# Kernel tuning notes

Measured on AMD Instinct MI355X. Metric: run time of the kernel, lower is better.

Reference implementation:

```python
import jax, jax.numpy as jnp
import numpy as np

H = 64  # hidden_size


def lstm_layer(x, Wih, Whh, bih, bhh):
    """Single LSTM layer, batch_first input x: [B, T, D]. Returns (hs [B,T,H], h_last [B,H]).
    PyTorch gate order: i, f, g, o."""
    B, T, _ = x.shape
    # Precompute input projections for all timesteps: [T, B, 4H]
    xg = jnp.einsum('btd,gd->tbg', x, Wih) + (bih + bhh)

    def step(carry, xt):
        h, c = carry
        gates = xt + h @ Whh.T  # [B, 4H]
        i, f, g, o = jnp.split(gates, 4, axis=-1)
        i = jax.nn.sigmoid(i)
        f = jax.nn.sigmoid(f)
        g = jnp.tanh(g)
        o = jax.nn.sigmoid(o)
        c = f * c + i * g
        h = o * jnp.tanh(c)
        return (h, c), h

    h0 = jnp.zeros((B, H), dtype=x.dtype)
    c0 = jnp.zeros((B, H), dtype=x.dtype)
    (h_last, _), hs = jax.lax.scan(step, (h0, c0), xg)
    return jnp.transpose(hs, (1, 0, 2)), h_last  # [B,T,H], [B,H]


def setup_inputs() -> dict:
    key = jax.random.key(0)
    ks = jax.random.split(key, 11)
    B, T, D = 1024, 512, 6
    s0 = 1.0 / np.sqrt(H)
    u = lambda k, shp: jax.random.uniform(k, shp, jnp.float32, -s0, s0)
    return {
        'x': jax.random.normal(ks[0], (B, T, D), jnp.float32),
        'Wih0': u(ks[1], (4 * H, D)),
        'Whh0': u(ks[2], (4 * H, H)),
        'bih0': u(ks[3], (4 * H,)),
        'bhh0': u(ks[4], (4 * H,)),
        'Wih1': u(ks[5], (4 * H, H)),
        'Whh1': u(ks[6], (4 * H, H)),
        'bih1': u(ks[7], (4 * H,)),
        'bhh1': u(ks[8], (4 * H,)),
        'W1': u(ks[9], (32, H)),
        'b1': jnp.zeros((32,), jnp.float32),
        'W2': u(ks[10], (1, 32)),
        'b2': jnp.zeros((1,), jnp.float32),
    }


def reference(x, Wih0, Whh0, bih0, bhh0, Wih1, Whh1, bih1, bhh1, W1, b1, W2, b2):
    # Layer 0 (dropout between layers is identity in eval mode)
    hs0, _ = lstm_layer(x, Wih0, Whh0, bih0, bhh0)
    # Layer 1: only last hidden state needed
    _, h_last = lstm_layer(hs0, Wih1, Whh1, bih1, bhh1)
    # MLP head: Linear -> ReLU -> (Dropout=identity) -> Linear -> Sigmoid
    z = jax.nn.relu(h_last @ W1.T + b1)
    out = jax.nn.sigmoid(z @ W2.T + b2)
    return out.squeeze()  # [B]
```

## Files before the change

kernel.cpp:

```cpp
#include <hip/hip_runtime.h>
#include <cstdint>

#define Hh 64
#define Tt 512
#define Dd 6
#define BB 4
#define NT 512

typedef short bf16x8 __attribute__((ext_vector_type(8)));
typedef float f32x4  __attribute__((ext_vector_type(4)));

#define MF(A, B, C) C = __builtin_amdgcn_mfma_f32_16x16x32_bf16(A, B, C, 0, 0, 0)

__device__ __forceinline__ float sigm(float v){
  return __builtin_amdgcn_rcpf(1.f + __expf(-v));
}
__device__ __forceinline__ float tanh_(float v){
  return 1.f - 2.f*__builtin_amdgcn_rcpf(1.f + __expf(2.f*v));
}
__device__ __forceinline__ unsigned short f2bf(float f){
  union { float f; unsigned u; } v; v.f = f;
  unsigned r = v.u + 0x7FFFu + ((v.u >> 16) & 1u);
  return (unsigned short)(r >> 16);
}
__device__ __forceinline__ float bf2f(unsigned short b){
  union { unsigned u; float f; } v; v.u = ((unsigned)b) << 16;
  return v.f;
}
__device__ __forceinline__ void split8(const float* w, bf16x8& hi, bf16x8& lo){
  #pragma unroll
  for (int i = 0; i < 8; ++i){
    unsigned short h_ = f2bf(w[i]);
    hi[i] = (short)h_;
    lo[i] = (short)f2bf(w[i] - bf2f(h_));
  }
}

__global__ __launch_bounds__(NT, 2)
void lstm2_mfma(const float* __restrict__ x,
                const float* __restrict__ Wih0, const float* __restrict__ Whh0,
                const float* __restrict__ bih0, const float* __restrict__ bhh0,
                const float* __restrict__ Wih1, const float* __restrict__ Whh1,
                const float* __restrict__ bih1, const float* __restrict__ bhh1,
                const float* __restrict__ W1, const float* __restrict__ b1,
                const float* __restrict__ W2, const float* __restrict__ b2,
                float* __restrict__ out)
{
  __shared__ __align__(16) short hsb[2*2*1024];
  __shared__ __align__(16) float h1f[BB*Hh];
  __shared__ float zs[BB*32];

  const int tid  = threadIdx.x;
  const int lane = tid & 63;
  const int wid  = tid >> 6;
  const int lr   = lane & 15;
  const int lg   = lane >> 4;
  const int b0   = blockIdx.x * BB;

  const int u_l  = lr >> 3;
  const int u_p  = (lr >> 2) & 1;
  const int u_bs = lr & 3;
  const int u_j  = wid*8 + u_p*4 + lg;

  {
    int* hz = (int*)hsb;
    hz[tid] = 0; hz[tid+NT] = 0; hz[tid+2*NT] = 0; hz[tid+3*NT] = 0;
  }

  bf16x8 A0[2][2][2];
  bf16x8 A1[2][2][2][2];
  #pragma unroll
  for (int p = 0; p < 2; ++p){
    const int m = (lr&3)*64 + wid*8 + p*4 + (lr>>2);
    #pragma unroll
    for (int kt = 0; kt < 2; ++kt){
      const int off = m*64 + kt*32 + lg*8;
      float wbuf[8];
      *(float4*)&wbuf[0] = *(const float4*)&Whh0[off];
      *(float4*)&wbuf[4] = *(const float4*)&Whh0[off+4];
      split8(wbuf, A0[p][kt][0], A0[p][kt][1]);
      *(float4*)&wbuf[0] = *(const float4*)&Wih1[off];
      *(float4*)&wbuf[4] = *(const float4*)&Wih1[off+4];
      split8(wbuf, A1[p][0][kt][0], A1[p][0][kt][1]);
      *(float4*)&wbuf[0] = *(const float4*)&Whh1[off];
      *(float4*)&wbuf[4] = *(const float4*)&Whh1[off+4];
      split8(wbuf, A1[p][1][kt][0], A1[p][1][kt][1]);
    }
  }

  float bias_g[4], w0r[24];
  #pragma unroll
  for (int gt = 0; gt < 4; ++gt){
    const int row = gt*64 + u_j;
    if (u_l == 0){
      bias_g[gt] = bih0[row] + bhh0[row];
      #pragma unroll
      for (int d = 0; d < Dd; ++d) w0r[gt*6+d] = Wih0[row*Dd + d];
    } else {
      bias_g[gt] = bih1[row] + bhh1[row];
      #pragma unroll
      for (int d = 0; d < Dd; ++d) w0r[gt*6+d] = 0.f;
    }
  }

  const int boff0 = (lr*128 + lg*16)      ^ ((lr&7)<<4);
  const int boff1 = (lr*128 + 64 + lg*16) ^ ((lr&7)<<4);
  const int whi   = (u_bs*128     + u_j*2) ^ (u_bs<<4);
  const int wlo   = ((u_bs+4)*128 + u_j*2) ^ ((u_bs+4)<<4);

  const float2* px2 = (const float2*)(x + (size_t)(b0 + u_bs) * (Tt*Dd));
  float2 xi0 = px2[0], xi1 = px2[1], xi2 = px2[2];
  float2 xc0 = px2[3], xc1 = px2[4], xc2 = px2[5];
  float2 xf0 = px2[6], xf1 = px2[7], xf2 = px2[8];

  float creg = 0.f;
  __syncthreads();

  if (u_l == 0){
    float s[4];
    #pragma unroll
    for (int gt = 0; gt < 4; ++gt)
      s[gt] = bias_g[gt] + w0r[gt*6+0]*xi0.x + w0r[gt*6+1]*xi0.y
            + w0r[gt*6+2]*xi1.x + w0r[gt*6+3]*xi1.y
            + w0r[gt*6+4]*xi2.x + w0r[gt*6+5]*xi2.y;
    float iv = sigm(s[0]), fv = sigm(s[1]), gv = tanh_(s[2]), ov = sigm(s[3]);
    creg = fv*creg + iv*gv;
    float hval = ov * tanh_(creg);
    unsigned short hh = f2bf(hval);
    unsigned short hl = f2bf(hval - bf2f(hh));
    char* hw = (char*)hsb;
    *(short*)(hw + whi) = (short)hh;
    *(short*)(hw + wlo) = (short)hl;
  }
  __syncthreads();

  #pragma unroll 2
  for (int t = 0; t < Tt; ++t){
    float2 xn0, xn1, xn2;
    {
      const int tl = (t+3 < Tt) ? (t+3) : (Tt-1);
      xn0 = px2[tl*3]; xn1 = px2[tl*3+1]; xn2 = px2[tl*3+2];
    }

    const int buf = t & 1;
    const char* hb = (const char*)hsb + buf*4096;
    bf16x8 b00 = *(const bf16x8*)(hb + boff0);
    bf16x8 b01 = *(const bf16x8*)(hb + boff1);
    bf16x8 b10 = *(const bf16x8*)(hb + 2048 + boff0);
    bf16x8 b11 = *(const bf16x8*)(hb + 2048 + boff1);

    f32x4 a00 = {0,0,0,0}, a01 = {0,0,0,0}, a10 = {0,0,0,0}, a11 = {0,0,0,0};
    MF(A0[0][0][0], b00, a00); MF(A0[1][0][0], b00, a01);
    MF(A0[0][1][0], b01, a00); MF(A0[1][1][0], b01, a01);
    MF(A0[0][0][1], b00, a00); MF(A0[1][0][1], b00, a01);
    MF(A0[0][1][1], b01, a00); MF(A0[1][1][1], b01, a01);

    float g0[4];
    #pragma unroll
    for (int rg = 0; rg < 4; ++rg){
      float own = (lr & 4) ? a01[rg] : a00[rg];
      float snd = (lr & 4) ? a00[rg] : a01[rg];
      g0[rg] = own + __shfl_xor(snd, 4);
    }

    MF(A1[0][0][0][0], b00, a10); MF(A1[1][0][0][0], b00, a11);
    MF(A1[0][0][1][0], b01, a10); MF(A1[1][0][1][0], b01, a11);
    MF(A1[0][0][0][1], b00, a10); MF(A1[1][0][0][1], b00, a11);
    MF(A1[0][0][1][1], b01, a10); MF(A1[1][0][1][1], b01, a11);
    MF(A1[0][1][0][0], b10, a10); MF(A1[1][1][0][0], b10, a11);
    MF(A1[0][1][1][0], b11, a10); MF(A1[1][1][1][0], b11, a11);
    MF(A1[0][1][0][1], b10, a10); MF(A1[1][1][0][1], b10, a11);
    MF(A1[0][1][1][1], b11, a10); MF(A1[1][1][1][1], b11, a11);

    float g1[4];
    #pragma unroll
    for (int rg = 0; rg < 4; ++rg){
      float s10 = a10[rg] + __shfl_xor(a10[rg], 4);
      float s11 = a11[rg] + __shfl_xor(a11[rg], 4);
      float snd = (lr & 4) ? s11 : s10;
      g1[rg] = __shfl_xor(snd, 8);
    }

    if ((u_l == 1) | (t+1 < Tt)){
      float s0 = ((u_l == 0) ? g0[0] : g1[0]) + bias_g[0];
      float s1 = ((u_l == 0) ? g0[1] : g1[1]) + bias_g[1];
      float s2 = ((u_l == 0) ? g0[2] : g1[2]) + bias_g[2];
      float s3 = ((u_l == 0) ? g0[3] : g1[3]) + bias_g[3];
      if (u_l == 0){
        s0 += w0r[ 0]*xc0.x + w0r[ 1]*xc0.y + w0r[ 2]*xc1.x
            + w0r[ 3]*xc1.y + w0r[ 4]*xc2.x + w0r[ 5]*xc2.y;
        s1 += w0r[ 6]*xc0.x + w0r[ 7]*xc0.y + w0r[ 8]*xc1.x
            + w0r[ 9]*xc1.y + w0r[10]*xc2.x + w0r[11]*xc2.y;
        s2 += w0r[12]*xc0.x + w0r[13]*xc0.y + w0r[14]*xc1.x
            + w0r[15]*xc1.y + w0r[16]*xc2.x + w0r[17]*xc2.y;
        s3 += w0r[18]*xc0.x + w0r[19]*xc0.y + w0r[20]*xc1.x
            + w0r[21]*xc1.y + w0r[22]*xc2.x + w0r[23]*xc2.y;
      }
      float iv = sigm(s0), fv = sigm(s1), gv = tanh_(s2), ov = sigm(s3);
      creg = fv*creg + iv*gv;
      float hval = ov * tanh_(creg);
      if ((u_l == 1) & (t == Tt-1)) h1f[u_bs*64 + u_j] = hval;
      unsigned short hh = f2bf(hval);
      unsigned short hl = f2bf(hval - bf2f(hh));
      char* hw = (char*)hsb + (buf^1)*4096 + u_l*2048;
      *(short*)(hw + whi) = (short)hh;
      *(short*)(hw + wlo) = (short)hl;
    }

    xc0 = xf0; xc1 = xf1; xc2 = xf2;
    xf0 = xn0; xf1 = xn1; xf2 = xn2;

    __syncthreads();
  }

  if (tid < BB*32){
    const int bsh = tid >> 5, m = tid & 31;
    float acc = b1[m];
    #pragma unroll
    for (int j = 0; j < Hh; ++j) acc += W1[m*Hh + j] * h1f[bsh*64 + j];
    zs[bsh*32 + m] = fmaxf(acc, 0.f);
  }
  __syncthreads();
  if (tid < BB){
    float acc = b2[0];
    #pragma unroll
    for (int m = 0; m < 32; ++m) acc += W2[m] * zs[tid*32 + m];
    out[b0 + tid] = sigm(acc);
  }
}

extern "C" void kernel_launch(void* const* d_in, const int* in_sizes, int n_in,
                              void* d_out, int out_size, void* d_ws, size_t ws_size,
                              hipStream_t stream) {
  const float* x    = (const float*)d_in[0];
  const float* Wih0 = (const float*)d_in[1];
  const float* Whh0 = (const float*)d_in[2];
  const float* bih0 = (const float*)d_in[3];
  const float* bhh0 = (const float*)d_in[4];
  const float* Wih1 = (const float*)d_in[5];
  const float* Whh1 = (const float*)d_in[6];
  const float* bih1 = (const float*)d_in[7];
  const float* bhh1 = (const float*)d_in[8];
  const float* W1   = (const float*)d_in[9];
  const float* b1   = (const float*)d_in[10];
  const float* W2   = (const float*)d_in[11];
  const float* b2   = (const float*)d_in[12];

  const int B = in_sizes[0] / (Tt*Dd);
  dim3 grid(B / BB), block(NT);
  hipLaunchKernelGGL(lstm2_mfma, grid, block, 0, stream,
                     x, Wih0, Whh0, bih0, bhh0, Wih1, Whh1, bih1, bhh1,
                     W1, b1, W2, b2, (float*)d_out);
}
```

Before: 436.0 us.

## Halve block to four waves, each lane computing both LSTM layers' units

Cuts the block from 512 to 256 threads. Each wave now owns 16 hidden units instead of 8 and holds weight fragments for both layers. Every lane runs the cell update for layer 0 and layer 1, instead of splitting lanes between layers. Layer-1 input and recurrent products go into separate accumulators and are summed before the cross-lane shuffle reduction. The aim is fewer waves taking part in each per-timestep barrier and less lane divergence, at the cost of more register pressure (launch bounds lowered to 1) and more serial MFMA and transcendental work per wave.

After: 770.0 us. +76.6%, slower.

```diff
diff --git a/kernel.cpp b/kernel.cpp
--- a/kernel.cpp
+++ b/kernel.cpp
@@ -5,7 +5,7 @@
 #define Tt 512
 #define Dd 6
 #define BB 4
-#define NT 512
+#define NT 256
 
 typedef short bf16x8 __attribute__((ext_vector_type(8)));
 typedef float f32x4  __attribute__((ext_vector_type(4)));
@@ -36,7 +36,7 @@
   }
 }
 
-__global__ __launch_bounds__(NT, 2)
+__global__ __launch_bounds__(NT, 1)
 void lstm2_mfma(const float* __restrict__ x,
                 const float* __restrict__ Wih0, const float* __restrict__ Whh0,
                 const float* __restrict__ bih0, const float* __restrict__ bhh0,
@@ -55,23 +55,24 @@
   const int wid  = tid >> 6;
   const int lr   = lane & 15;
   const int lg   = lane >> 4;
+  const int sb2  = (lr >> 2) & 1;
+  const int sb3  = lr >> 3;
+  const int u_bs = lr & 3;
+  const int u_j  = wid*16 + (2*sb3 + sb2)*4 + lg;
   const int b0   = blockIdx.x * BB;
-
-  const int u_l  = lr >> 3;
-  const int u_p  = (lr >> 2) & 1;
-  const int u_bs = lr & 3;
-  const int u_j  = wid*8 + u_p*4 + lg;
 
   {
     int* hz = (int*)hsb;
-    hz[tid] = 0; hz[tid+NT] = 0; hz[tid+2*NT] = 0; hz[tid+3*NT] = 0;
-  }
-
-  bf16x8 A0[2][2][2];
-  bf16x8 A1[2][2][2][2];
+    #pragma unroll
+    for (int i = 0; i < 8; ++i) hz[tid + i*NT] = 0;
+  }
+
+  bf16x8 A0[4][2][2];
+  bf16x8 A1i[4][2][2];
+  bf16x8 A1h[4][2][2];
   #pragma unroll
-  for (int p = 0; p < 2; ++p){
-    const int m = (lr&3)*64 + wid*8 + p*4 + (lr>>2);
+  for (int p = 0; p < 4; ++p){
+    const int m = (lr&3)*64 + wid*16 + p*4 + (lr>>2);
     #pragma unroll
     for (int kt = 0; kt < 2; ++kt){
       const int off = m*64 + kt*32 + lg*8;
@@ -81,26 +82,21 @@
       split8(wbuf, A0[p][kt][0], A0[p][kt][1]);
       *(float4*)&wbuf[0] = *(const float4*)&Wih1[off];
       *(float4*)&wbuf[4] = *(const float4*)&Wih1[off+4];
-      split8(wbuf, A1[p][0][kt][0], A1[p][0][kt][1]);
+      split8(wbuf, A1i[p][kt][0], A1i[p][kt][1]);
       *(float4*)&wbuf[0] = *(const float4*)&Whh1[off];
       *(float4*)&wbuf[4] = *(const float4*)&Whh1[off+4];
-      split8(wbuf, A1[p][1][kt][0], A1[p][1][kt][1]);
-    }
-  }
-
-  float bias_g[4], w0r[24];
+      split8(wbuf, A1h[p][kt][0], A1h[p][kt][1]);
+    }
+  }
+
+  float bias0g[4], bias1g[4], w0r[24];
   #pragma unroll
   for (int gt = 0; gt < 4; ++gt){
     const int row = gt*64 + u_j;
-    if (u_l == 0){
-      bias_g[gt] = bih0[row] + bhh0[row];
-      #pragma unroll
-      for (int d = 0; d < Dd; ++d) w0r[gt*6+d] = Wih0[row*Dd + d];
-    } else {
-      bias_g[gt] = bih1[row] + bhh1[row];
-      #pragma unroll
-      for (int d = 0; d < Dd; ++d) w0r[gt*6+d] = 0.f;
-    }
+    bias0g[gt] = bih0[row] + bhh0[row];
+    bias1g[gt] = bih1[row] + bhh1[row];
+    #pragma unroll
+    for (int d = 0; d < Dd; ++d) w0r[gt*6+d] = Wih0[row*Dd + d];
   }
 
   const int boff0 = (lr*128 + lg*16)      ^ ((lr&7)<<4);
@@ -113,19 +109,19 @@
   float2 xc0 = px2[3], xc1 = px2[4], xc2 = px2[5];
   float2 xf0 = px2[6], xf1 = px2[7], xf2 = px2[8];
 
-  float creg = 0.f;
+  float c0reg = 0.f, c1reg = 0.f;
   __syncthreads();
 
-  if (u_l == 0){
+  {
     float s[4];
     #pragma unroll
     for (int gt = 0; gt < 4; ++gt)
-      s[gt] = bias_g[gt] + w0r[gt*6+0]*xi0.x + w0r[gt*6+1]*xi0.y
+      s[gt] = bias0g[gt] + w0r[gt*6+0]*xi0.x + w0r[gt*6+1]*xi0.y
             + w0r[gt*6+2]*xi1.x + w0r[gt*6+3]*xi1.y
             + w0r[gt*6+4]*xi2.x + w0r[gt*6+5]*xi2.y;
     float iv = sigm(s[0]), fv = sigm(s[1]), gv = tanh_(s[2]), ov = sigm(s[3]);
-    creg = fv*creg + iv*gv;
-    float hval = ov * tanh_(creg);
+    c0reg = fv*c0reg + iv*gv;
+    float hval = ov * tanh_(c0reg);
     unsigned short hh = f2bf(hval);
     unsigned short hl = f2bf(hval - bf2f(hh));
     char* hw = (char*)hsb;
@@ -149,60 +145,89 @@
     bf16x8 b10 = *(const bf16x8*)(hb + 2048 + boff0);
     bf16x8 b11 = *(const bf16x8*)(hb + 2048 + boff1);
 
-    f32x4 a00 = {0,0,0,0}, a01 = {0,0,0,0}, a10 = {0,0,0,0}, a11 = {0,0,0,0};
-    MF(A0[0][0][0], b00, a00); MF(A0[1][0][0], b00, a01);
-    MF(A0[0][1][0], b01, a00); MF(A0[1][1][0], b01, a01);
-    MF(A0[0][0][1], b00, a00); MF(A0[1][0][1], b00, a01);
-    MF(A0[0][1][1], b01, a00); MF(A0[1][1][1], b01, a01);
-
-    float g0[4];
+    f32x4 a0_[4], a1i_[4], a1h_[4];
+    #pragma unroll
+    for (int p = 0; p < 4; ++p){
+      a0_[p] = (f32x4){0,0,0,0}; a1i_[p] = (f32x4){0,0,0,0}; a1h_[p] = (f32x4){0,0,0,0};
+    }
+    #pragma unroll
+    for (int p = 0; p < 4; ++p){
+      MF(A0[p][0][0], b00, a0_[p]);
+      MF(A0[p][1][0], b01, a0_[p]);
+      MF(A0[p][0][1], b00, a0_[p]);
+      MF(A0[p][1][1], b01, a0_[p]);
+    }
+    #pragma unroll
+    for (int p = 0; p < 4; ++p){
+      MF(A1i[p][0][0], b00, a1i_[p]);
+      MF(A1i[p][1][0], b01, a1i_[p]);
+      MF(A1i[p][0][1], b00, a1i_[p]);
+      MF(A1i[p][1][1], b01, a1i_[p]);
+    }
+    #pragma unroll
+    for (int p = 0; p < 4; ++p){
+      MF(A1h[p][0][0], b10, a1h_[p]);
+      MF(A1h[p][1][0], b11, a1h_[p]);
+      MF(A1h[p][0][1], b10, a1h_[p]);
+      MF(A1h[p][1][1], b11, a1h_[p]);
+    }
+
+    float g0[4], g1[4];
     #pragma unroll
     for (int rg = 0; rg < 4; ++rg){
-      float own = (lr & 4) ? a01[rg] : a00[rg];
-      float snd = (lr & 4) ? a00[rg] : a01[rg];
-      g0[rg] = own + __shfl_xor(snd, 4);
-    }
-
-    MF(A1[0][0][0][0], b00, a10); MF(A1[1][0][0][0], b00, a11);
-    MF(A1[0][0][1][0], b01, a10); MF(A1[1][0][1][0], b01, a11);
-    MF(A1[0][0][0][1], b00, a10); MF(A1[1][0][0][1], b00, a11);
-    MF(A1[0][0][1][1], b01, a10); MF(A1[1][0][1][1], b01, a11);
-    MF(A1[0][1][0][0], b10, a10); MF(A1[1][1][0][0], b10, a11);
-    MF(A1[0][1][1][0], b11, a10); MF(A1[1][1][1][0], b11, a11);
-    MF(A1[0][1][0][1], b10, a10); MF(A1[1][1][0][1], b10, a11);
-    MF(A1[0][1][1][1], b11, a10); MF(A1[1][1][1][1], b11, a11);
-
-    float g1[4];
-    #pragma unroll
-    for (int rg = 0; rg < 4; ++rg){
-      float s10 = a10[rg] + __shfl_xor(a10[rg], 4);
-      float s11 = a11[rg] + __shfl_xor(a11[rg], 4);
-      float snd = (lr & 4) ? s11 : s10;
-      g1[rg] = __shfl_xor(snd, 8);
-    }
-
-    if ((u_l == 1) | (t+1 < Tt)){
-      float s0 = ((u_l == 0) ? g0[0] : g1[0]) + bias_g[0];
-      float s1 = ((u_l == 0) ? g0[1] : g1[1]) + bias_g[1];
-      float s2 = ((u_l == 0) ? g0[2] : g1[2]) + bias_g[2];
-      float s3 = ((u_l == 0) ? g0[3] : g1[3]) + bias_g[3];
-      if (u_l == 0){
-        s0 += w0r[ 0]*xc0.x + w0r[ 1]*xc0.y + w0r[ 2]*xc1.x
-            + w0r[ 3]*xc1.y + w0r[ 4]*xc2.x + w0r[ 5]*xc2.y;
-        s1 += w0r[ 6]*xc0.x + w0r[ 7]*xc0.y + w0r[ 8]*xc1.x
-            + w0r[ 9]*xc1.y + w0r[10]*xc2.x + w0r[11]*xc2.y;
-        s2 += w0r[12]*xc0.x + w0r[13]*xc0.y + w0r[14]*xc1.x
-            + w0r[15]*xc1.y + w0r[16]*xc2.x + w0r[17]*xc2.y;
-        s3 += w0r[18]*xc0.x + w0r[19]*xc0.y + w0r[20]*xc1.x
-            + w0r[21]*xc1.y + w0r[22]*xc2.x + w0r[23]*xc2.y;
-      }
+      float own  = sb2 ? a0_[1][rg] : a0_[0][rg];
+      float snd  = sb2 ? a0_[0][rg] : a0_[1][rg];
+      float own2 = sb2 ? a0_[3][rg] : a0_[2][rg];
+      float snd2 = sb2 ? a0_[2][rg] : a0_[3][rg];
+      float f  = own  + __shfl_xor(snd, 4);
+      float f2 = own2 + __shfl_xor(snd2, 4);
+      g0[rg] = sb3 ? __shfl_xor(f2, 8) : f;
+      float m0 = a1i_[0][rg] + a1h_[0][rg];
+      float m1 = a1i_[1][rg] + a1h_[1][rg];
+      float m2 = a1i_[2][rg] + a1h_[2][rg];
+      float m3 = a1i_[3][rg] + a1h_[3][rg];
+      float o1  = sb2 ? m1 : m0, s1_ = sb2 ? m0 : m1;
+      float o2_ = sb2 ? m3 : m2, s2_ = sb2 ? m2 : m3;
+      float h_  = o1  + __shfl_xor(s1_, 4);
+      float h2_ = o2_ + __shfl_xor(s2_, 4);
+      g1[rg] = sb3 ? __shfl_xor(h2_, 8) : h_;
+    }
+
+    if (t+1 < Tt){
+      float s0 = g0[0] + bias0g[0]
+               + w0r[ 0]*xc0.x + w0r[ 1]*xc0.y + w0r[ 2]*xc1.x
+               + w0r[ 3]*xc1.y + w0r[ 4]*xc2.x + w0r[ 5]*xc2.y;
+      float s1 = g0[1] + bias0g[1]
+               + w0r[ 6]*xc0.x + w0r[ 7]*xc0.y + w0r[ 8]*xc1.x
+               + w0r[ 9]*xc1.y + w0r[10]*xc2.x + w0r[11]*xc2.y;
+      float s2 = g0[2] + bias0g[2]
+               + w0r[12]*xc0.x + w0r[13]*xc0.y + w0r[14]*xc1.x
+               + w0r[15]*xc1.y + w0r[16]*xc2.x + w0r[17]*xc2.y;
+      float s3 = g0[3] + bias0g[3]
+               + w0r[18]*xc0.x + w0r[19]*xc0.y + w0r[20]*xc1.x
+               + w0r[21]*xc1.y + w0r[22]*xc2.x + w0r[23]*xc2.y;
       float iv = sigm(s0), fv = sigm(s1), gv = tanh_(s2), ov = sigm(s3);
-      creg = fv*creg + iv*gv;
-      float hval = ov * tanh_(creg);
-      if ((u_l == 1) & (t == Tt-1)) h1f[u_bs*64 + u_j] = hval;
+      c0reg = fv*c0reg + iv*gv;
+      float hval = ov * tanh_(c0reg);
       unsigned short hh = f2bf(hval);
       unsigned short hl = f2bf(hval - bf2f(hh));
-      char* hw = (char*)hsb + (buf^1)*4096 + u_l*2048;
+      char* hw = (char*)hsb + (buf^1)*4096;
+      *(short*)(hw + whi) = (short)hh;
+      *(short*)(hw + wlo) = (short)hl;
+    }
+
+    {
+      float s0 = g1[0] + bias1g[0];
+      float s1 = g1[1] + bias1g[1];
+      float s2 = g1[2] + bias1g[2];
+      float s3 = g1[3] + bias1g[3];
+      float iv = sigm(s0), fv = sigm(s1), gv = tanh_(s2), ov = sigm(s3);
+      c1reg = fv*c1reg + iv*gv;
+      float hval = ov * tanh_(c1reg);
+      if (t == Tt-1) h1f[u_bs*64 + u_j] = hval;
+      unsigned short hh = f2bf(hval);
+      unsigned short hl = f2bf(hval - bf2f(hh));
+      char* hw = (char*)hsb + (buf^1)*4096 + 2048;
       *(short*)(hw + whi) = (short)hh;
       *(short*)(hw + wlo) = (short)hl;
     }
```

## Process eight sequences per block with 16 waves and split gate work across lanes

Applied to the files above, without the earlier changes.

Doubles the batch per block to 8 sequences and the block to 1024 threads, with each wave owning 4 hidden units instead of 8. Per-wave MFMA work drops to 12 instructions per step in three independent accumulator chains, and the input projection is split across lane halves and exchanged with a shuffle. The aim is a shorter serial latency per timestep on the recurrent critical path. The cost is half as many blocks, occupancy limited to one block per CU, and a barrier across 16 waves each step.

Result: slower. 577.5 us (+32.4%).

```diff
diff --git a/kernel.cpp b/kernel.cpp
--- a/kernel.cpp
+++ b/kernel.cpp
@@ -4,8 +4,8 @@
 #define Hh 64
 #define Tt 512
 #define Dd 6
-#define BB 4
-#define NT 512
+#define BB 8
+#define NT 1024
 
 typedef short bf16x8 __attribute__((ext_vector_type(8)));
 typedef float f32x4  __attribute__((ext_vector_type(4)));
@@ -36,7 +36,7 @@
   }
 }
 
-__global__ __launch_bounds__(NT, 2)
+__global__ __launch_bounds__(NT, 1)
 void lstm2_mfma(const float* __restrict__ x,
                 const float* __restrict__ Wih0, const float* __restrict__ Whh0,
                 const float* __restrict__ bih0, const float* __restrict__ bhh0,
@@ -55,82 +55,82 @@
   const int wid  = tid >> 6;
   const int lr   = lane & 15;
   const int lg   = lane >> 4;
+  const int u_l  = (lane >> 3) & 1;
+  const int u_bs = lane & 7;
+  const int u_j  = wid*4 + lg;
   const int b0   = blockIdx.x * BB;
-
-  const int u_l  = lr >> 3;
-  const int u_p  = (lr >> 2) & 1;
-  const int u_bs = lr & 3;
-  const int u_j  = wid*8 + u_p*4 + lg;
 
   {
     int* hz = (int*)hsb;
-    hz[tid] = 0; hz[tid+NT] = 0; hz[tid+2*NT] = 0; hz[tid+3*NT] = 0;
-  }
-
-  bf16x8 A0[2][2][2];
-  bf16x8 A1[2][2][2][2];
-  #pragma unroll
-  for (int p = 0; p < 2; ++p){
-    const int m = (lr&3)*64 + wid*8 + p*4 + (lr>>2);
+    #pragma unroll
+    for (int i = 0; i < 4; ++i) hz[tid + i*NT] = 0;
+  }
+
+  bf16x8 A0[2][2];
+  bf16x8 A1i[2][2];
+  bf16x8 A1h[2][2];
+  {
+    const int m = (lr&3)*64 + wid*4 + (lr>>2);
     #pragma unroll
     for (int kt = 0; kt < 2; ++kt){
       const int off = m*64 + kt*32 + lg*8;
       float wbuf[8];
       *(float4*)&wbuf[0] = *(const float4*)&Whh0[off];
       *(float4*)&wbuf[4] = *(const float4*)&Whh0[off+4];
-      split8(wbuf, A0[p][kt][0], A0[p][kt][1]);
+      split8(wbuf, A0[kt][0], A0[kt][1]);
       *(float4*)&wbuf[0] = *(const float4*)&Wih1[off];
       *(float4*)&wbuf[4] = *(const float4*)&Wih1[off+4];
-      split8(wbuf, A1[p][0][kt][0], A1[p][0][kt][1]);
+      split8(wbuf, A1i[kt][0], A1i[kt][1]);
       *(float4*)&wbuf[0] = *(const float4*)&Whh1[off];
       *(float4*)&wbuf[4] = *(const float4*)&Whh1[off+4];
-      split8(wbuf, A1[p][1][kt][0], A1[p][1][kt][1]);
-    }
-  }
-
-  float bias_g[4], w0r[24];
+      split8(wbuf, A1h[kt][0], A1h[kt][1]);
+    }
+  }
+
+  float bias_g[4], w0r[12];
   #pragma unroll
   for (int gt = 0; gt < 4; ++gt){
     const int row = gt*64 + u_j;
-    if (u_l == 0){
-      bias_g[gt] = bih0[row] + bhh0[row];
-      #pragma unroll
-      for (int d = 0; d < Dd; ++d) w0r[gt*6+d] = Wih0[row*Dd + d];
-    } else {
-      bias_g[gt] = bih1[row] + bhh1[row];
-      #pragma unroll
-      for (int d = 0; d < Dd; ++d) w0r[gt*6+d] = 0.f;
-    }
+    bias_g[gt] = (u_l == 0) ? (bih0[row] + bhh0[row]) : (bih1[row] + bhh1[row]);
+  }
+  #pragma unroll
+  for (int e = 0; e < 2; ++e){
+    const int row = (2*u_l + e)*64 + u_j;
+    #pragma unroll
+    for (int d = 0; d < Dd; ++d) w0r[e*6+d] = Wih0[row*Dd + d];
   }
 
   const int boff0 = (lr*128 + lg*16)      ^ ((lr&7)<<4);
   const int boff1 = (lr*128 + 64 + lg*16) ^ ((lr&7)<<4);
   const int whi   = (u_bs*128     + u_j*2) ^ (u_bs<<4);
-  const int wlo   = ((u_bs+4)*128 + u_j*2) ^ ((u_bs+4)<<4);
+  const int wlo   = ((u_bs+8)*128 + u_j*2) ^ (u_bs<<4);
 
   const float2* px2 = (const float2*)(x + (size_t)(b0 + u_bs) * (Tt*Dd));
-  float2 xi0 = px2[0], xi1 = px2[1], xi2 = px2[2];
   float2 xc0 = px2[3], xc1 = px2[4], xc2 = px2[5];
   float2 xf0 = px2[6], xf1 = px2[7], xf2 = px2[8];
 
   float creg = 0.f;
   __syncthreads();
 
-  if (u_l == 0){
-    float s[4];
-    #pragma unroll
-    for (int gt = 0; gt < 4; ++gt)
-      s[gt] = bias_g[gt] + w0r[gt*6+0]*xi0.x + w0r[gt*6+1]*xi0.y
-            + w0r[gt*6+2]*xi1.x + w0r[gt*6+3]*xi1.y
-            + w0r[gt*6+4]*xi2.x + w0r[gt*6+5]*xi2.y;
-    float iv = sigm(s[0]), fv = sigm(s[1]), gv = tanh_(s[2]), ov = sigm(s[3]);
-    creg = fv*creg + iv*gv;
-    float hval = ov * tanh_(creg);
-    unsigned short hh = f2bf(hval);
-    unsigned short hl = f2bf(hval - bf2f(hh));
-    char* hw = (char*)hsb;
-    *(short*)(hw + whi) = (short)hh;
-    *(short*)(hw + wlo) = (short)hl;
+  {
+    float2 xi0 = px2[0], xi1 = px2[1], xi2 = px2[2];
+    float xpA = w0r[0]*xi0.x + w0r[1]*xi0.y + w0r[2]*xi1.x
+              + w0r[3]*xi1.y + w0r[4]*xi2.x + w0r[5]*xi2.y;
+    float xpB = w0r[6]*xi0.x + w0r[7]*xi0.y + w0r[8]*xi1.x
+              + w0r[9]*xi1.y + w0r[10]*xi2.x + w0r[11]*xi2.y;
+    float r2 = __shfl_xor(xpA, 8), r3 = __shfl_xor(xpB, 8);
+    if (u_l == 0){
+      float s0 = bias_g[0] + xpA, s1 = bias_g[1] + xpB;
+      float s2 = bias_g[2] + r2,  s3 = bias_g[3] + r3;
+      float iv = sigm(s0), fv = sigm(s1), gv = tanh_(s2), ov = sigm(s3);
+      creg = fv*creg + iv*gv;
+      float hval = ov * tanh_(creg);
+      unsigned short hh = f2bf(hval);
+      unsigned short hl = f2bf(hval - bf2f(hh));
+      char* hw = (char*)hsb;
+      *(short*)(hw + whi) = (short)hh;
+      *(short*)(hw + wlo) = (short)hl;
+    }
   }
   __syncthreads();
 
@@ -149,53 +149,33 @@
     bf16x8 b10 = *(const bf16x8*)(hb + 2048 + boff0);
     bf16x8 b11 = *(const bf16x8*)(hb + 2048 + boff1);
 
-    f32x4 a00 = {0,0,0,0}, a01 = {0,0,0,0}, a10 = {0,0,0,0}, a11 = {0,0,0,0};
-    MF(A0[0][0][0], b00, a00); MF(A0[1][0][0], b00, a01);
-    MF(A0[0][1][0], b01, a00); MF(A0[1][1][0], b01, a01);
-    MF(A0[0][0][1], b00, a00); MF(A0[1][0][1], b00, a01);
-    MF(A0[0][1][1], b01, a00); MF(A0[1][1][1], b01, a01);
-
-    float g0[4];
-    #pragma unroll
-    for (int rg = 0; rg < 4; ++rg){
-      float own = (lr & 4) ? a01[rg] : a00[rg];
-      float snd = (lr & 4) ? a00[rg] : a01[rg];
-      g0[rg] = own + __shfl_xor(snd, 4);
-    }
-
-    MF(A1[0][0][0][0], b00, a10); MF(A1[1][0][0][0], b00, a11);
-    MF(A1[0][0][1][0], b01, a10); MF(A1[1][0][1][0], b01, a11);
-    MF(A1[0][0][0][1], b00, a10); MF(A1[1][0][0][1], b00, a11);
-    MF(A1[0][0][1][1], b01, a10); MF(A1[1][0][1][1], b01, a11);
-    MF(A1[0][1][0][0], b10, a10); MF(A1[1][1][0][0], b10, a11);
-    MF(A1[0][1][1][0], b11, a10); MF(A1[1][1][1][0], b11, a11);
-    MF(A1[0][1][0][1], b10, a10); MF(A1[1][1][0][1], b10, a11);
-    MF(A1[0][1][1][1], b11, a10); MF(A1[1][1][1][1], b11, a11);
-
-    float g1[4];
-    #pragma unroll
-    for (int rg = 0; rg < 4; ++rg){
-      float s10 = a10[rg] + __shfl_xor(a10[rg], 4);
-      float s11 = a11[rg] + __shfl_xor(a11[rg], 4);
-      float snd = (lr & 4) ? s11 : s10;
-      g1[rg] = __shfl_xor(snd, 8);
-    }
+    f32x4 a0 = {0,0,0,0}, a1i = {0,0,0,0}, a1h = {0,0,0,0};
+    MF(A0[0][0], b00, a0);  MF(A1i[0][0], b00, a1i);  MF(A1h[0][0], b10, a1h);
+    MF(A0[1][0], b01, a0);  MF(A1i[1][0], b01, a1i);  MF(A1h[1][0], b11, a1h);
+    MF(A0[0][1], b00, a0);  MF(A1i[0][1], b00, a1i);  MF(A1h[0][1], b10, a1h);
+    MF(A0[1][1], b01, a0);  MF(A1i[1][1], b01, a1i);  MF(A1h[1][1], b11, a1h);
+
+    float xpA = w0r[0]*xc0.x + w0r[1]*xc0.y + w0r[2]*xc1.x
+              + w0r[3]*xc1.y + w0r[4]*xc2.x + w0r[5]*xc2.y;
+    float xpB = w0r[6]*xc0.x + w0r[7]*xc0.y + w0r[8]*xc1.x
+              + w0r[9]*xc1.y + w0r[10]*xc2.x + w0r[11]*xc2.y;
+    float r2 = __shfl_xor(xpA, 8), r3 = __shfl_xor(xpB, 8);
+
+    float s0, s1, s2, s3;
+    {
+      float m0 = a1i[0] + a1h[0], m1 = a1i[1] + a1h[1],
+            m2 = a1i[2] + a1h[2], m3 = a1i[3] + a1h[3];
+      float q0 = u_l ? m0 : a0[0], q1 = u_l ? m1 : a0[1],
+            q2 = u_l ? m2 : a0[2], q3 = u_l ? m3 : a0[3];
+      s0 = q0 + __shfl_xor(u_l ? m0 : a0[0], 8);
+      s1 = q1 + __shfl_xor(u_l ? m1 : a0[1], 8);
+      s2 = q2 + __shfl_xor(u_l ? m2 : a0[2], 8);
+      s3 = q3 + __shfl_xor(u_l ? m3 : a0[3], 8);
+    }
+    s0 += bias_g[0]; s1 += bias_g[1]; s2 += bias_g[2]; s3 += bias_g[3];
+    if (u_l == 0){ s0 += xpA; s1 += xpB; s2 += r2; s3 += r3; }
 
     if ((u_l == 1) | (t+1 < Tt)){
-      float s0 = ((u_l == 0) ? g0[0] : g1[0]) + bias_g[0];
-      float s1 = ((u_l == 0) ? g0[1] : g1[1]) + bias_g[1];
-      float s2 = ((u_l == 0) ? g0[2] : g1[2]) + bias_g[2];
-      float s3 = ((u_l == 0) ? g0[3] : g1[3]) + bias_g[3];
-      if (u_l == 0){
-        s0 += w0r[ 0]*xc0.x + w0r[ 1]*xc0.y + w0r[ 2]*xc1.x
-            + w0r[ 3]*xc1.y + w0r[ 4]*xc2.x + w0r[ 5]*xc2.y;
-        s1 += w0r[ 6]*xc0.x + w0r[ 7]*xc0.y + w0r[ 8]*xc1.x
-            + w0r[ 9]*xc1.y + w0r[10]*xc2.x + w0r[11]*xc2.y;
-        s2 += w0r[12]*xc0.x + w0r[13]*xc0.y + w0r[14]*xc1.x
-            + w0r[15]*xc1.y + w0r[16]*xc2.x + w0r[17]*xc2.y;
-        s3 += w0r[18]*xc0.x + w0r[19]*xc0.y + w0r[20]*xc1.x
-            + w0r[21]*xc1.y + w0r[22]*xc2.x + w0r[23]*xc2.y;
-      }
       float iv = sigm(s0), fv = sigm(s1), gv = tanh_(s2), ov = sigm(s3);
       creg = fv*creg + iv*gv;
       float hval = ov * tanh_(creg);
```

## Issue all MFMAs upfront, split layer gate paths, truncate bf16 split, lighter barrier

Applied to the files above, without the earlier changes.

Issues both layers' MFMAs together and splits the layer-1 accumulators into separate input and hidden chains, so the layer-0 reduction and gate math can overlap with the layer-1 MFMAs. The layer-0 and layer-1 gate evaluations become separate branches instead of one select-based shared path. The rounding bf16 hi/lo split becomes plain truncation, and the loop barrier becomes an inline s_waitcnt lgkmcnt(0) plus s_barrier. Launch bounds drop from 2 to 1 block per SM, which gives more registers per thread but may lower occupancy.

New measurement: 540.0 us. 23.9% more time.

```diff
diff --git a/kernel.cpp b/kernel.cpp
--- a/kernel.cpp
+++ b/kernel.cpp
@@ -35,8 +35,15 @@
     lo[i] = (short)f2bf(w[i] - bf2f(h_));
   }
 }
-
-__global__ __launch_bounds__(NT, 2)
+__device__ __forceinline__ void splitH(float v, unsigned short& hh, unsigned short& hl){
+  union { float f; unsigned u; } a; a.f = v;
+  hh = (unsigned short)(a.u >> 16);
+  float resid = v - bf2f(hh);
+  union { float f; unsigned u; } b; b.f = resid;
+  hl = (unsigned short)(b.u >> 16);
+}
+
+__global__ __launch_bounds__(NT, 1)
 void lstm2_mfma(const float* __restrict__ x,
                 const float* __restrict__ Wih0, const float* __restrict__ Whh0,
                 const float* __restrict__ bih0, const float* __restrict__ bhh0,
@@ -126,8 +133,7 @@
     float iv = sigm(s[0]), fv = sigm(s[1]), gv = tanh_(s[2]), ov = sigm(s[3]);
     creg = fv*creg + iv*gv;
     float hval = ov * tanh_(creg);
-    unsigned short hh = f2bf(hval);
-    unsigned short hl = f2bf(hval - bf2f(hh));
+    unsigned short hh, hl; splitH(hval, hh, hl);
     char* hw = (char*)hsb;
     *(short*)(hw + whi) = (short)hh;
     *(short*)(hw + wlo) = (short)hl;
@@ -149,11 +155,22 @@
     bf16x8 b10 = *(const bf16x8*)(hb + 2048 + boff0);
     bf16x8 b11 = *(const bf16x8*)(hb + 2048 + boff1);
 
-    f32x4 a00 = {0,0,0,0}, a01 = {0,0,0,0}, a10 = {0,0,0,0}, a11 = {0,0,0,0};
+    f32x4 a00  = {0,0,0,0}, a01  = {0,0,0,0};
+    f32x4 a1iA = {0,0,0,0}, a1iB = {0,0,0,0};
+    f32x4 a1hA = {0,0,0,0}, a1hB = {0,0,0,0};
+
     MF(A0[0][0][0], b00, a00); MF(A0[1][0][0], b00, a01);
     MF(A0[0][1][0], b01, a00); MF(A0[1][1][0], b01, a01);
     MF(A0[0][0][1], b00, a00); MF(A0[1][0][1], b00, a01);
     MF(A0[0][1][1], b01, a00); MF(A0[1][1][1], b01, a01);
+    MF(A1[0][0][0][0], b00, a1iA); MF(A1[1][0][0][0], b00, a1iB);
+    MF(A1[0][0][1][0], b01, a1iA); MF(A1[1][0][1][0], b01, a1iB);
+    MF(A1[0][0][0][1], b00, a1iA); MF(A1[1][0][0][1], b00, a1iB);
+    MF(A1[0][0][1][1], b01, a1iA); MF(A1[1][0][1][1], b01, a1iB);
+    MF(A1[0][1][0][0], b10, a1hA); MF(A1[1][1][0][0], b10, a1hB);
+    MF(A1[0][1][1][0], b11, a1hA); MF(A1[1][1][1][0], b11, a1hB);
+    MF(A1[0][1][0][1], b10, a1hA); MF(A1[1][1][0][1], b10, a1hB);
+    MF(A1[0][1][1][1], b11, a1hA); MF(A1[1][1][1][1], b11, a1hB);
 
     float g0[4];
     #pragma unroll
@@ -162,56 +179,60 @@
       float snd = (lr & 4) ? a00[rg] : a01[rg];
       g0[rg] = own + __shfl_xor(snd, 4);
     }
-
-    MF(A1[0][0][0][0], b00, a10); MF(A1[1][0][0][0], b00, a11);
-    MF(A1[0][0][1][0], b01, a10); MF(A1[1][0][1][0], b01, a11);
-    MF(A1[0][0][0][1], b00, a10); MF(A1[1][0][0][1], b00, a11);
-    MF(A1[0][0][1][1], b01, a10); MF(A1[1][0][1][1], b01, a11);
-    MF(A1[0][1][0][0], b10, a10); MF(A1[1][1][0][0], b10, a11);
-    MF(A1[0][1][1][0], b11, a10); MF(A1[1][1][1][0], b11, a11);
-    MF(A1[0][1][0][1], b10, a10); MF(A1[1][1][0][1], b10, a11);
-    MF(A1[0][1][1][1], b11, a10); MF(A1[1][1][1][1], b11, a11);
-
-    float g1[4];
-    #pragma unroll
-    for (int rg = 0; rg < 4; ++rg){
-      float s10 = a10[rg] + __shfl_xor(a10[rg], 4);
-      float s11 = a11[rg] + __shfl_xor(a11[rg], 4);
-      float snd = (lr & 4) ? s11 : s10;
-      g1[rg] = __shfl_xor(snd, 8);
-    }
-
-    if ((u_l == 1) | (t+1 < Tt)){
-      float s0 = ((u_l == 0) ? g0[0] : g1[0]) + bias_g[0];
-      float s1 = ((u_l == 0) ? g0[1] : g1[1]) + bias_g[1];
-      float s2 = ((u_l == 0) ? g0[2] : g1[2]) + bias_g[2];
-      float s3 = ((u_l == 0) ? g0[3] : g1[3]) + bias_g[3];
-      if (u_l == 0){
-        s0 += w0r[ 0]*xc0.x + w0r[ 1]*xc0.y + w0r[ 2]*xc1.x
-            + w0r[ 3]*xc1.y + w0r[ 4]*xc2.x + w0r[ 5]*xc2.y;
-        s1 += w0r[ 6]*xc0.x + w0r[ 7]*xc0.y + w0r[ 8]*xc1.x
-            + w0r[ 9]*xc1.y + w0r[10]*xc2.x + w0r[11]*xc2.y;
-        s2 += w0r[12]*xc0.x + w0r[13]*xc0.y + w0r[14]*xc1.x
-            + w0r[15]*xc1.y + w0r[16]*xc2.x + w0r[17]*xc2.y;
-        s3 += w0r[18]*xc0.x + w0r[19]*xc0.y + w0r[20]*xc1.x
-            + w0r[21]*xc1.y + w0r[22]*xc2.x + w0r[23]*xc2.y;
-      }
+    if ((u_l == 0) & (t+1 < Tt)){
+      float s0 = g0[0] + bias_g[0]
+               + w0r[ 0]*xc0.x + w0r[ 1]*xc0.y + w0r[ 2]*xc1.x
+               + w0r[ 3]*xc1.y + w0r[ 4]*xc2.x + w0r[ 5]*xc2.y;
+      float s1 = g0[1] + bias_g[1]
+               + w0r[ 6]*xc0.x + w0r[ 7]*xc0.y + w0r[ 8]*xc1.x
+               + w0r[ 9]*xc1.y + w0r[10]*xc2.x + w0r[11]*xc2.y;
+      float s2 = g0[2] + bias_g[2]
+               + w0r[12]*xc0.x + w0r[13]*xc0.y + w0r[14]*xc1.x
+               + w0r[15]*xc1.y + w0r[16]*xc2.x + w0r[17]*xc2.y;
+      float s3 = g0[3] + bias_g[3]
+               + w0r[18]*xc0.x + w0r[19]*xc0.y + w0r[20]*xc1.x
+               + w0r[21]*xc1.y + w0r[22]*xc2.x + w0r[23]*xc2.y;
       float iv = sigm(s0), fv = sigm(s1), gv = tanh_(s2), ov = sigm(s3);
       creg = fv*creg + iv*gv;
       float hval = ov * tanh_(creg);
-      if ((u_l == 1) & (t == Tt-1)) h1f[u_bs*64 + u_j] = hval;
-      unsigned short hh = f2bf(hval);
-      unsigned short hl = f2bf(hval - bf2f(hh));
-      char* hw = (char*)hsb + (buf^1)*4096 + u_l*2048;
+      unsigned short hh, hl; splitH(hval, hh, hl);
+      char* hw = (char*)hsb + (buf^1)*4096;
       *(short*)(hw + whi) = (short)hh;
       *(short*)(hw + wlo) = (short)hl;
     }
 
+    float g1[4];
+    #pragma unroll
+    for (int rg = 0; rg < 4; ++rg){
+      float m0 = a1iA[rg] + a1hA[rg];
+      float m1 = a1iB[rg] + a1hB[rg];
+      float s10 = m0 + __shfl_xor(m0, 4);
+      float s11 = m1 + __shfl_xor(m1, 4);
+      float snd = (lr & 4) ? s11 : s10;
+      g1[rg] = __shfl_xor(snd, 8);
+    }
+    if (u_l == 1){
+      float s0 = g1[0] + bias_g[0];
+      float s1 = g1[1] + bias_g[1];
+      float s2 = g1[2] + bias_g[2];
+      float s3 = g1[3] + bias_g[3];
+      float iv = sigm(s0), fv = sigm(s1), gv = tanh_(s2), ov = sigm(s3);
+      creg = fv*creg + iv*gv;
+      float hval = ov * tanh_(creg);
+      if (t == Tt-1) h1f[u_bs*64 + u_j] = hval;
+      unsigned short hh, hl; splitH(hval, hh, hl);
+      char* hw = (char*)hsb + (buf^1)*4096 + 2048;
+      *(short*)(hw + whi) = (short)hh;
+      *(short*)(hw + wlo) = (short)hl;
+    }
+
     xc0 = xf0; xc1 = xf1; xc2 = xf2;
     xf0 = xn0; xf1 = xn1; xf2 = xn2;
 
-    __syncthreads();
-  }
+    asm volatile("s_waitcnt lgkmcnt(0)\n\ts_barrier" ::: "memory");
+  }
+
+  __syncthreads();
 
   if (tid < BB*32){
     const int bsh = tid >> 5, m = tid & 31;
```
